# Kernel tuning notes

Hardware: AMD Instinct MI355X
Metric: run time of the kernel (lower is better)

The kernel has to match this reference:

```python
import jax, jax.numpy as jnp
import numpy as np

N, E, B, DIM, NF, EF, HID = 50000, 100000, 2000, 64, 14, 4, 128


def setup_inputs() -> dict:
    key = jax.random.key(0)
    ks = jax.random.split(key, 30)
    rn = lambda k, shape, scale: jax.random.normal(k, shape, jnp.float32) * scale
    inp = {}
    inp["x"] = rn(ks[0], (N, NF), 1.0)
    inp["edge_attr"] = jax.random.uniform(ks[1], (E, EF), jnp.float32)
    inp["edge_index"] = jax.random.randint(ks[2], (2, E), 0, N)
    # equal-size graphs: 25 nodes per graph, sorted segment ids
    inp["batch"] = (jnp.arange(N, dtype=jnp.int32) // (N // B)).astype(jnp.int32)
    inp["lin0_w"] = rn(ks[3], (DIM, NF), (1.0 / NF) ** 0.5)
    inp["lin0_b"] = jnp.zeros((DIM,), jnp.float32)
    inp["mlp_w1"] = rn(ks[4], (HID, EF), (1.0 / EF) ** 0.5)
    inp["mlp_b1"] = jnp.zeros((HID,), jnp.float32)
    inp["mlp_w2"] = rn(ks[5], (DIM * DIM, HID), (1.0 / HID) ** 0.5)
    inp["mlp_b2"] = jnp.zeros((DIM * DIM,), jnp.float32)
    inp["root"] = rn(ks[6], (DIM, DIM), (1.0 / DIM) ** 0.5)
    inp["conv_b"] = jnp.zeros((DIM,), jnp.float32)
    inp["gru_wih"] = rn(ks[7], (3 * DIM, DIM), (1.0 / DIM) ** 0.5)
    inp["gru_whh"] = rn(ks[8], (3 * DIM, DIM), (1.0 / DIM) ** 0.5)
    inp["gru_bih"] = jnp.zeros((3 * DIM,), jnp.float32)
    inp["gru_bhh"] = jnp.zeros((3 * DIM,), jnp.float32)
    inp["lstm_wih"] = rn(ks[9], (4 * DIM, 2 * DIM), (1.0 / (2 * DIM)) ** 0.5)
    inp["lstm_whh"] = rn(ks[10], (4 * DIM, DIM), (1.0 / DIM) ** 0.5)
    inp["lstm_bih"] = jnp.zeros((4 * DIM,), jnp.float32)
    inp["lstm_bhh"] = jnp.zeros((4 * DIM,), jnp.float32)
    inp["lin1_w"] = rn(ks[11], (DIM, 2 * DIM), (1.0 / (2 * DIM)) ** 0.5)
    inp["lin1_b"] = jnp.zeros((DIM,), jnp.float32)
    inp["lin2_w"] = rn(ks[12], (1, DIM), (1.0 / DIM) ** 0.5)
    inp["lin2_b"] = jnp.zeros((1,), jnp.float32)
    return inp


def _forward(x, edge_attr, edge_index, batch, lin0_w, lin0_b, mlp_w1, mlp_b1,
             mlp_w2, mlp_b2, root, conv_b, gru_wih, gru_whh, gru_bih, gru_bhh,
             lstm_wih, lstm_whh, lstm_bih, lstm_bhh, lin1_w, lin1_b, lin2_w, lin2_b):
    src, dst = edge_index[0], edge_index[1]
    n = x.shape[0]
    # edge MLP -> per-edge weight matrices [E, DIM, DIM]
    h_e = jax.nn.relu(edge_attr @ mlp_w1.T + mlp_b1)
    W_e = (h_e @ mlp_w2.T + mlp_b2).reshape(-1, DIM, DIM)
    deg = jnp.clip(jax.ops.segment_sum(jnp.ones_like(dst, jnp.float32), dst, n), 1.0)

    out = jax.nn.relu(x @ lin0_w.T + lin0_b)
    h = out  # GRU hidden (seq_len=1, 1 layer)
    for _ in range(3):
        msg = jnp.einsum('ei,eio->eo', out[src], W_e)  # per-edge matmul
        agg = jax.ops.segment_sum(msg, dst, n) / deg[:, None]  # scatter-mean
        m = jax.nn.relu(agg + out @ root + conv_b)  # NNConv: aggr + root + bias
        # GRU step
        gi = m @ gru_wih.T + gru_bih
        gh = h @ gru_whh.T + gru_bhh
        i_r, i_z, i_n = jnp.split(gi, 3, axis=-1)
        h_r, h_z, h_n = jnp.split(gh, 3, axis=-1)
        r = jax.nn.sigmoid(i_r + h_r)
        z = jax.nn.sigmoid(i_z + h_z)
        ng = jnp.tanh(i_n + r * h_n)
        h = (1.0 - z) * ng + z * h
        out = h

    # Set2Set pooling, 3 processing steps
    b = B
    qh = jnp.zeros((b, DIM), out.dtype)
    qc = jnp.zeros((b, DIM), out.dtype)
    q_star = jnp.zeros((b, 2 * DIM), out.dtype)
    for _ in range(3):
        gates = q_star @ lstm_wih.T + lstm_bih + qh @ lstm_whh.T + lstm_bhh
        gi_, gf_, gg_, go_ = jnp.split(gates, 4, axis=-1)
        qc = jax.nn.sigmoid(gf_) * qc + jax.nn.sigmoid(gi_) * jnp.tanh(gg_)
        qh = jax.nn.sigmoid(go_) * jnp.tanh(qc)
        q = qh
        e = jnp.sum(out * q[batch], axis=-1)  # [N]
        e_max = jax.ops.segment_max(e, batch, b)
        a = jnp.exp(e - e_max[batch])
        denom = jax.ops.segment_sum(a, batch, b)
        a = a / denom[batch]
        r_read = jax.ops.segment_sum(a[:, None] * out, batch, b)
        q_star = jnp.concatenate([q, r_read], axis=-1)

    y = jax.nn.relu(q_star @ lin1_w.T + lin1_b)
    y = y @ lin2_w.T + lin2_b
    return y.reshape(-1)


def reference(x, edge_attr, edge_index, batch, lin0_w, lin0_b, mlp_w1, mlp_b1,
              mlp_w2, mlp_b2, root, conv_b, gru_wih, gru_whh, gru_bih, gru_bhh,
              lstm_wih, lstm_whh, lstm_bih, lstm_bhh, lin1_w, lin1_b, lin2_w, lin2_b):
    return _forward(x, edge_attr, edge_index, batch, lin0_w, lin0_b, mlp_w1, mlp_b1,
                    mlp_w2, mlp_b2, root, conv_b, gru_wih, gru_whh, gru_bih, gru_bhh,
                    lstm_wih, lstm_whh, lstm_bih, lstm_bhh, lin1_w, lin1_b, lin2_w, lin2_b)
```

## Files before the change

### kernel.cpp

```cpp
#include <hip/hip_runtime.h>
#include <hip/hip_bf16.h>

#define NN 50000
#define EE 100000
#define BB 2000
#define DIM 64
#define NF 14
#define EF 4
#define HID 128
#define EPAD 100096

typedef __attribute__((ext_vector_type(8))) _Float16 half8;
typedef __attribute__((ext_vector_type(4))) _Float16 half4;
typedef __attribute__((ext_vector_type(4))) float floatx4;

__device__ __forceinline__ void async16(const _Float16* g, _Float16* l) {
    __builtin_amdgcn_global_load_lds(
        (const __attribute__((address_space(1))) unsigned int*)g,
        (__attribute__((address_space(3))) unsigned int*)l,
        16, 0, 0);
}

__global__ void prep_weights_kernel(
    const float* __restrict__ lih, const float* __restrict__ lhh, const float* __restrict__ l1,
    const float* __restrict__ root, const float* __restrict__ b2,
    const float* __restrict__ wih, const float* __restrict__ whh,
    const float* __restrict__ bih, const float* __restrict__ bhh,
    const float* __restrict__ w2,
    float* __restrict__ lihT, float* __restrict__ lhhT, float* __restrict__ l1T,
    _Float16* __restrict__ W1h, _Float16* __restrict__ W2h, float* __restrict__ fbias,
    _Float16* __restrict__ W2rT) {
    int t = blockIdx.x * 256 + threadIdx.x;
    if (t < 64 * 8192) {
        int o = t >> 13, k = t & 8191, i = k >> 7, h = k & 127;
        W2rT[(size_t)o * 8192 + k] = (_Float16)w2[(size_t)(i * 64 + o) * 128 + h];
    }
    if (t < 256 * 128) { int j = t / 128, k = t % 128; lihT[k * 256 + j] = lih[t]; }
    if (t < 256 * 64) { int j = t / 64, k = t % 64; lhhT[k * 256 + j] = lhh[t]; }
    if (t < 64 * 128) { int d = t / 128, k = t % 128; l1T[k * 64 + d] = l1[t]; }
    if (t < 64 * 128) {
        int n = t >> 7, k = t & 127;
        W1h[t] = (_Float16)(k < 64 ? root[k * 64 + n] : b2[(size_t)(k - 64) * 64 + n]);
    }
    if (t < 256 * 128) {
        int n2 = t >> 7, k = t & 127;
        int g = n2 >> 6, j = n2 & 63;
        float v;
        if (g == 0)      v = (k < 64) ? wih[j * 64 + k]         : whh[j * 64 + (k - 64)];
        else if (g == 1) v = (k < 64) ? wih[(64 + j) * 64 + k]  : whh[(64 + j) * 64 + (k - 64)];
        else if (g == 2) v = (k < 64) ? wih[(128 + j) * 64 + k] : 0.f;
        else             v = (k < 64) ? 0.f                     : whh[(128 + j) * 64 + (k - 64)];
        W2h[t] = (_Float16)v;
    }
    if (t < 256) {
        int g = t >> 6, j = t & 63;
        float v = (g == 0) ? bih[j] + bhh[j]
                : (g == 1) ? bih[64 + j] + bhh[64 + j]
                : (g == 2) ? bih[128 + j] : bhh[128 + j];
        fbias[t] = v;
    }
}

__global__ void prep_ne_kernel(const float* __restrict__ ea, const float* __restrict__ w1,
                               const float* __restrict__ b1, _Float16* __restrict__ he,
                               const float* __restrict__ x, const float* __restrict__ l0w,
                               const float* __restrict__ l0b, float* __restrict__ hv,
                               const int* __restrict__ ei, float* __restrict__ deg) {
    int t = blockIdx.x * 256 + threadIdx.x;
    if (t < EPAD * 128) {
        int el = t >> 7, h = t & 127;
        float acc = 0.f;
        if (el < EE) {
            const float4 a = *(const float4*)(ea + (size_t)el * 4);
            const float4 w = *(const float4*)(w1 + h * 4);
            acc = fmaxf(b1[h] + a.x * w.x + a.y * w.y + a.z * w.z + a.w * w.w, 0.f);
        }
        he[t] = (_Float16)acc;
    }
    if (t < NN * 64) {
        int n = t >> 6, d = t & 63;
        float acc = l0b[d];
        #pragma unroll
        for (int f = 0; f < NF; f++) acc += x[n * NF + f] * l0w[d * NF + f];
        hv[t] = fmaxf(acc, 0.f);
    }
    if (t < EE) atomicAdd(&deg[ei[EE + t]], 1.0f);
}

__global__ __launch_bounds__(256, 2) void msg_gemm_kernel(
    const float* __restrict__ hv, const _Float16* __restrict__ he16,
    const _Float16* __restrict__ W2rT, const int* __restrict__ ei,
    float* __restrict__ agg, float* __restrict__ xsum) {
    __shared__ _Float16 sB[2][16 * 64 * 8];
    __shared__ _Float16 sXs[256 * 72];
    __shared__ int sDst[256];
    const int t = threadIdx.x;
    const int eb = blockIdx.x * 256;
    const int lane = t & 63;
    const int w = t >> 6;
    const int col = lane & 15;
    const int quad = lane >> 4;

    if (t < 256) {
        int e = eb + t;
        sDst[t] = (e < EE) ? ei[EE + e] : 0;
    }
    #pragma unroll 4
    for (int rep = 0; rep < 16; rep++) {
        int idx = rep * 256 + t;
        int el = idx >> 4, d4 = idx & 15;
        int e = eb + el;
        float4 v = {0.f, 0.f, 0.f, 0.f};
        if (e < EE) {
            int src = ei[e];
            v = *(const float4*)(hv + (size_t)src * 64 + d4 * 4);
        }
        half4 h4 = {(_Float16)v.x, (_Float16)v.y, (_Float16)v.z, (_Float16)v.w};
        *(half4*)&sXs[el * 72 + d4 * 4] = h4;
    }
    __syncthreads();

    #pragma unroll 4
    for (int rep = 0; rep < 64; rep++) {
        int idx = rep * 256 + t;
        int el = idx >> 6, d = idx & 63;
        if (eb + el < EE)
            atomicAdd(&xsum[(size_t)sDst[el] * 64 + d], (float)sXs[el * 72 + d]);
    }

    half8 heReg[4][4];
    #pragma unroll
    for (int mt = 0; mt < 4; mt++) {
        int row = eb + w * 64 + mt * 16 + col;
        #pragma unroll
        for (int p = 0; p < 4; p++)
            heReg[mt][p] = *(const half8*)(he16 + (size_t)row * 128 + p * 32 + quad * 8);
    }

    floatx4 Cacc[4][4];
    #pragma unroll
    for (int mt = 0; mt < 4; mt++)
        #pragma unroll
        for (int nt = 0; nt < 4; nt++)
            Cacc[mt][nt] = (floatx4){0.f, 0.f, 0.f, 0.f};

    const _Float16* gsrc = W2rT + (size_t)(w * 16 + col) * 8192 + quad * 8;
    #pragma unroll
    for (int rep = 0; rep < 4; rep++)
        async16(gsrc + rep * 32, &sB[0][((w * 4 + rep) * 64 + lane) * 8]);
    __syncthreads();

    #pragma unroll 1
    for (int i4 = 0; i4 < 16; i4++) {
        half4 xsv[4];
        #pragma unroll
        for (int mt = 0; mt < 4; mt++)
            xsv[mt] = *(const half4*)&sXs[(w * 64 + mt * 16 + col) * 72 + i4 * 4];
        #pragma unroll
        for (int ii = 0; ii < 4; ii++) {
            const int i = i4 * 4 + ii;
            const int buf = i & 1;
            if (i < 63) {
                #pragma unroll
                for (int rep = 0; rep < 4; rep++)
                    async16(gsrc + (size_t)(i + 1) * 128 + rep * 32,
                            &sB[buf ^ 1][((w * 4 + rep) * 64 + lane) * 8]);
            }
            #pragma unroll
            for (int ks = 0; ks < 4; ks++) {
                half8 bfr[4];
                #pragma unroll
                for (int nt = 0; nt < 4; nt++)
                    bfr[nt] = *(const half8*)&sB[buf][((nt * 4 + ks) * 64 + lane) * 8];
                #pragma unroll
                for (int mt = 0; mt < 4; mt++) {
                    half8 afr = heReg[mt][ks] * xsv[mt][ii];
                    #pragma unroll
                    for (int nt = 0; nt < 4; nt++)
                        Cacc[mt][nt] = __builtin_amdgcn_mfma_f32_16x16x32_f16(afr, bfr[nt], Cacc[mt][nt], 0, 0, 0);
                }
            }
            __syncthreads();
        }
    }

    #pragma unroll
    for (int mt = 0; mt < 4; mt++) {
        #pragma unroll
        for (int r = 0; r < 4; r++) {
            int el = w * 64 + mt * 16 + quad * 4 + r;
            if (eb + el < EE) {
                float* ap = agg + (size_t)sDst[el] * 64 + col;
                #pragma unroll
                for (int nt = 0; nt < 4; nt++)
                    atomicAdd(ap + nt * 16, Cacc[mt][nt][r]);
            }
        }
    }
}

__global__ __launch_bounds__(256, 2) void node_fused_kernel(
    const float* __restrict__ hv_in, float* __restrict__ agg,
    float* __restrict__ xsum, const float* __restrict__ deg,
    const _Float16* __restrict__ W1h, const _Float16* __restrict__ W2h,
    const float* __restrict__ fbias, const float* __restrict__ cb,
    float* __restrict__ hv_out) {
    __shared__ _Float16 sA1[64 * 136];
    __shared__ _Float16 sA2[64 * 136];
    __shared__ float sH[64 * 68];
    __shared__ float sAgg[64 * 68];
    const int t = threadIdx.x;
    const int nb = blockIdx.x * 64;
    const int n = t >> 2, part = t & 3;
    {
        int gn = nb + n;
        bool valid = gn < NN;
        float inv = 1.f;
        if (valid) inv = 1.f / fmaxf(deg[gn], 1.f);
        #pragma unroll
        for (int c4 = 0; c4 < 4; c4++) {
            int d0 = part * 16 + c4 * 4;
            float4 hvv = {0.f, 0.f, 0.f, 0.f}, agv = {0.f, 0.f, 0.f, 0.f}, xsv = {0.f, 0.f, 0.f, 0.f};
            if (valid) {
                hvv = *(const float4*)(hv_in + (size_t)gn * 64 + d0);
                agv = *(const float4*)(agg + (size_t)gn * 64 + d0);
                xsv = *(const float4*)(xsum + (size_t)gn * 64 + d0);
            }
            agv.x *= inv; agv.y *= inv; agv.z *= inv; agv.w *= inv;
            xsv.x *= inv; xsv.y *= inv; xsv.z *= inv; xsv.w *= inv;
            half4 hvh = {(_Float16)hvv.x, (_Float16)hvv.y, (_Float16)hvv.z, (_Float16)hvv.w};
            half4 xsh = {(_Float16)xsv.x, (_Float16)xsv.y, (_Float16)xsv.z, (_Float16)xsv.w};
            *(half4*)&sA1[n * 136 + d0] = hvh;
            *(half4*)&sA1[n * 136 + 64 + d0] = xsh;
            *(half4*)&sA2[n * 136 + 64 + d0] = hvh;
            *(float4*)&sH[n * 68 + d0] = hvv;
            *(float4*)&sAgg[n * 68 + d0] = agv;
        }
        if (valid) {
            float4 z = {0.f, 0.f, 0.f, 0.f};
            #pragma unroll
            for (int c4 = 0; c4 < 4; c4++) {
                int d0 = part * 16 + c4 * 4;
                *(float4*)(agg + (size_t)gn * 64 + d0) = z;
                *(float4*)(xsum + (size_t)gn * 64 + d0) = z;
            }
        }
    }
    __syncthreads();

    const int lane = t & 63, w = t >> 6;
    const int col = lane & 15, quad = lane >> 4;

    floatx4 C1[4];
    #pragma unroll
    for (int nt = 0; nt < 4; nt++) {
        float b = cb[nt * 16 + col];
        C1[nt] = (floatx4){b, b, b, b};
    }
    #pragma unroll
    for (int ks = 0; ks < 4; ks++) {
        half8 a = *(const half8*)&sA1[(w * 16 + col) * 136 + ks * 32 + quad * 8];
        #pragma unroll
        for (int nt = 0; nt < 4; nt++) {
            half8 bfr = *(const half8*)(W1h + (size_t)(nt * 16 + col) * 128 + ks * 32 + quad * 8);
            C1[nt] = __builtin_amdgcn_mfma_f32_16x16x32_f16(a, bfr, C1[nt], 0, 0, 0);
        }
    }
    #pragma unroll
    for (int nt = 0; nt < 4; nt++) {
        #pragma unroll
        for (int r = 0; r < 4; r++) {
            int node = w * 16 + quad * 4 + r;
            int j = nt * 16 + col;
            float m = fmaxf(C1[nt][r] + sAgg[node * 68 + j], 0.f);
            sA2[node * 136 + j] = (_Float16)m;
        }
    }
    __syncthreads();

    floatx4 C2[16];
    #pragma unroll
    for (int nt2 = 0; nt2 < 16; nt2++) {
        float b = fbias[nt2 * 16 + col];
        C2[nt2] = (floatx4){b, b, b, b};
    }
    #pragma unroll
    for (int ks = 0; ks < 4; ks++) {
        half8 a = *(const half8*)&sA2[(w * 16 + col) * 136 + ks * 32 + quad * 8];
        #pragma unroll
        for (int nt2 = 0; nt2 < 16; nt2++) {
            half8 bfr = *(const half8*)(W2h + (size_t)(nt2 * 16 + col) * 128 + ks * 32 + quad * 8);
            C2[nt2] = __builtin_amdgcn_mfma_f32_16x16x32_f16(a, bfr, C2[nt2], 0, 0, 0);
        }
    }
    float hnew[4][4];
    #pragma unroll
    for (int r = 0; r < 4; r++) {
        int node = w * 16 + quad * 4 + r;
        #pragma unroll
        for (int jt = 0; jt < 4; jt++) {
            int j = jt * 16 + col;
            float rr = 1.f / (1.f + expf(-C2[jt][r]));
            float zz = 1.f / (1.f + expf(-C2[4 + jt][r]));
            float ng = tanhf(C2[8 + jt][r] + rr * C2[12 + jt][r]);
            float hold = sH[node * 68 + j];
            hnew[r][jt] = (1.f - zz) * ng + zz * hold;
        }
    }
    __syncthreads();
    #pragma unroll
    for (int r = 0; r < 4; r++) {
        int node = w * 16 + quad * 4 + r;
        #pragma unroll
        for (int jt = 0; jt < 4; jt++)
            sH[node * 68 + jt * 16 + col] = hnew[r][jt];
    }
    __syncthreads();
    {
        int gn = nb + n;
        if (gn < NN) {
            #pragma unroll
            for (int c4 = 0; c4 < 4; c4++) {
                int d0 = part * 16 + c4 * 4;
                *(float4*)(hv_out + (size_t)gn * 64 + d0) = *(const float4*)&sH[n * 68 + d0];
            }
        }
    }
}

__global__ __launch_bounds__(256) void set2set_kernel(
    const float* __restrict__ hv,
    const float* __restrict__ lihT, const float* __restrict__ lhhT,
    const float* __restrict__ l_bih, const float* __restrict__ l_bhh,
    const float* __restrict__ lin1T, const float* __restrict__ lin1_b,
    const float* __restrict__ lin2_w, const float* __restrict__ lin2_b,
    float* __restrict__ out) {
    __shared__ float outS[25 * 65];
    __shared__ float qs[128], qh[64], qc[64], gat[256], ew[32], aw[32], red[64];
    int g = blockIdx.x;
    int t = threadIdx.x;
    for (int p = t; p < 25 * 64; p += 256) {
        int j = p >> 6, i = p & 63;
        outS[j * 65 + i] = hv[(size_t)(g * 25 + j) * 64 + i];
    }
    if (t < 128) qs[t] = 0.f;
    if (t < 64) { qh[t] = 0.f; qc[t] = 0.f; }
    __syncthreads();
    for (int it = 0; it < 3; it++) {
        float acc = l_bih[t] + l_bhh[t];
        for (int k = 0; k < 128; k++) acc += qs[k] * lihT[k * 256 + t];
        for (int k = 0; k < 64; k++) acc += qh[k] * lhhT[k * 256 + t];
        gat[t] = acc;
        __syncthreads();
        if (t < 64) {
            float ig = 1.f / (1.f + expf(-gat[t]));
            float fg = 1.f / (1.f + expf(-gat[64 + t]));
            float gg = tanhf(gat[128 + t]);
            float og = 1.f / (1.f + expf(-gat[192 + t]));
            float c = fg * qc[t] + ig * gg;
            qc[t] = c;
            qh[t] = og * tanhf(c);
        }
        __syncthreads();
        if (t < 25) {
            float e = 0.f;
            for (int i = 0; i < 64; i++) e += outS[t * 65 + i] * qh[i];
            ew[t] = e;
        }
        __syncthreads();
        if (t == 0) {
            float mx = ew[0];
            for (int j = 1; j < 25; j++) mx = fmaxf(mx, ew[j]);
            float s = 0.f;
            for (int j = 0; j < 25; j++) { float a = expf(ew[j] - mx); aw[j] = a; s += a; }
            float inv = 1.f / s;
            for (int j = 0; j < 25; j++) aw[j] *= inv;
        }
        __syncthreads();
        if (t < 64) {
            float r = 0.f;
            for (int j = 0; j < 25; j++) r += aw[j] * outS[j * 65 + t];
            qs[t] = qh[t];
            qs[64 + t] = r;
        }
        __syncthreads();
    }
    if (t < 64) {
        float y1 = lin1_b[t];
        for (int k = 0; k < 128; k++) y1 += qs[k] * lin1T[k * 64 + t];
        y1 = fmaxf(y1, 0.f);
        red[t] = y1 * lin2_w[t];
    }
    __syncthreads();
    if (t == 0) {
        float y = lin2_b[0];
        for (int i = 0; i < 64; i++) y += red[i];
        out[g] = y;
    }
}

extern "C" void kernel_launch(void* const* d_in, const int* in_sizes, int n_in,
                              void* d_out, int out_size, void* d_ws, size_t ws_size,
                              hipStream_t stream) {
    const float* x        = (const float*)d_in[0];
    const float* ea       = (const float*)d_in[1];
    const int*   ei       = (const int*)  d_in[2];
    const float* lin0_w   = (const float*)d_in[4];
    const float* lin0_b   = (const float*)d_in[5];
    const float* mlp_w1   = (const float*)d_in[6];
    const float* mlp_b1   = (const float*)d_in[7];
    const float* mlp_w2   = (const float*)d_in[8];
    const float* mlp_b2   = (const float*)d_in[9];
    const float* root     = (const float*)d_in[10];
    const float* conv_b   = (const float*)d_in[11];
    const float* gru_wih  = (const float*)d_in[12];
    const float* gru_whh  = (const float*)d_in[13];
    const float* gru_bih  = (const float*)d_in[14];
    const float* gru_bhh  = (const float*)d_in[15];
    const float* lstm_wih = (const float*)d_in[16];
    const float* lstm_whh = (const float*)d_in[17];
    const float* lstm_bih = (const float*)d_in[18];
    const float* lstm_bhh = (const float*)d_in[19];
    const float* lin1_w   = (const float*)d_in[20];
    const float* lin1_b   = (const float*)d_in[21];
    const float* lin2_w   = (const float*)d_in[22];
    const float* lin2_b   = (const float*)d_in[23];
    float* out = (float*)d_out;

    char* base = (char*)d_ws;
    size_t off = 0;
    auto carve = [&](size_t bytes) -> void* {
        void* r = base + off;
        off = (off + bytes + 255) & ~(size_t)255;
        return r;
    };
    float* hv   = (float*)carve((size_t)NN * 64 * 4);
    float* agg  = (float*)carve((size_t)NN * 64 * 4);
    float* xsum = (float*)carve((size_t)NN * 64 * 4);
    float* deg  = (float*)carve((size_t)NN * 4);
    float* lihT = (float*)carve(128 * 256 * 4);
    float* lhhT = (float*)carve(64 * 256 * 4);
    float* l1T  = (float*)carve(128 * 64 * 4);
    float* fbias = (float*)carve(256 * 4);
    _Float16* he16 = (_Float16*)carve((size_t)EPAD * 128 * 2);
    _Float16* W2rT = (_Float16*)carve((size_t)64 * 8192 * 2);
    _Float16* W1h  = (_Float16*)carve((size_t)64 * 128 * 2);
    _Float16* W2h  = (_Float16*)carve((size_t)256 * 128 * 2);

    hipMemsetAsync(agg, 0, (size_t)NN * 64 * 4 * 2 + (size_t)NN * 4, stream);
    prep_weights_kernel<<<2048, 256, 0, stream>>>(lstm_wih, lstm_whh, lin1_w,
                                                  root, mlp_b2, gru_wih, gru_whh, gru_bih, gru_bhh,
                                                  mlp_w2, lihT, lhhT, l1T, W1h, W2h, fbias, W2rT);
    prep_ne_kernel<<<(EPAD * 128 + 255) / 256, 256, 0, stream>>>(ea, mlp_w1, mlp_b1, he16,
                                                                 x, lin0_w, lin0_b, hv, ei, deg);

    for (int it = 0; it < 3; it++) {
        msg_gemm_kernel<<<EPAD / 256, 256, 0, stream>>>(hv, he16, W2rT, ei, agg, xsum);
        node_fused_kernel<<<(NN + 63) / 64, 256, 0, stream>>>(hv, agg, xsum, deg,
                                                              W1h, W2h, fbias, conv_b, hv);
    }

    set2set_kernel<<<BB, 256, 0, stream>>>(hv, lihT, lhhT, lstm_bih, lstm_bhh,
                                           l1T, lin1_b, lin2_w, lin2_b, out);
}
```

Measured before the change: 813.8 us.

## Retile message GEMM warps to 128 edges by 32 columns with register-staged B loads

Each wave now covers 128 edges and 32 output columns instead of 64 edges and 64 columns. The weight loads change from global-to-LDS async copies to ordinary register prefetch, written to the other LDS buffer after the MFMAs run. The xsum atomic scatter moves after the GEMM, and the barrier before the he loads is dropped. This changes per-wave register use (heReg doubles), the LDS read pattern and the B-fragment reuse, and adds register pressure and possible occupancy loss under launch_bounds(256,2).

New measurement: 843.3 us. 3.6% more time.

```diff
diff --git a/kernel.cpp b/kernel.cpp
--- a/kernel.cpp
+++ b/kernel.cpp
@@ -13,13 +13,6 @@
 typedef __attribute__((ext_vector_type(8))) _Float16 half8;
 typedef __attribute__((ext_vector_type(4))) _Float16 half4;
 typedef __attribute__((ext_vector_type(4))) float floatx4;
-
-__device__ __forceinline__ void async16(const _Float16* g, _Float16* l) {
-    __builtin_amdgcn_global_load_lds(
-        (const __attribute__((address_space(1))) unsigned int*)g,
-        (__attribute__((address_space(3))) unsigned int*)l,
-        16, 0, 0);
-}
 
 __global__ void prep_weights_kernel(
     const float* __restrict__ lih, const float* __restrict__ lhh, const float* __restrict__ l1,
@@ -100,6 +93,8 @@
     const int w = t >> 6;
     const int col = lane & 15;
     const int quad = lane >> 4;
+    const int eh = w >> 1;
+    const int cg = w & 1;
 
     if (t < 256) {
         int e = eb + t;
@@ -118,84 +113,92 @@
         half4 h4 = {(_Float16)v.x, (_Float16)v.y, (_Float16)v.z, (_Float16)v.w};
         *(half4*)&sXs[el * 72 + d4 * 4] = h4;
     }
-    __syncthreads();
-
+
+    half8 heReg[8][4];
+    #pragma unroll
+    for (int mt = 0; mt < 8; mt++) {
+        int row = eb + eh * 128 + mt * 16 + col;
+        #pragma unroll
+        for (int p = 0; p < 4; p++)
+            heReg[mt][p] = *(const half8*)(he16 + (size_t)row * 128 + p * 32 + quad * 8);
+    }
+
+    floatx4 Cacc[8][2];
+    #pragma unroll
+    for (int mt = 0; mt < 8; mt++)
+        #pragma unroll
+        for (int nt = 0; nt < 2; nt++)
+            Cacc[mt][nt] = (floatx4){0.f, 0.f, 0.f, 0.f};
+
+    const _Float16* gsrc = W2rT + (size_t)((w >> 1) * 32 + (w & 1) * 16 + col) * 8192 + quad * 8;
+    half8 pre[4];
+    {
+        #pragma unroll
+        for (int rep = 0; rep < 4; rep++)
+            pre[rep] = *(const half8*)(gsrc + rep * 32);
+        #pragma unroll
+        for (int rep = 0; rep < 4; rep++)
+            *(half8*)&sB[0][((w * 4 + rep) * 64 + lane) * 8] = pre[rep];
+    }
+    __syncthreads();
+
+    #pragma unroll 1
+    for (int i4 = 0; i4 < 16; i4++) {
+        half4 xsv[8];
+        #pragma unroll
+        for (int mt = 0; mt < 8; mt++)
+            xsv[mt] = *(const half4*)&sXs[(eh * 128 + mt * 16 + col) * 72 + i4 * 4];
+        #pragma unroll
+        for (int ii = 0; ii < 4; ii++) {
+            const int i = i4 * 4 + ii;
+            const int buf = i & 1;
+            if (i < 63) {
+                #pragma unroll
+                for (int rep = 0; rep < 4; rep++)
+                    pre[rep] = *(const half8*)(gsrc + (size_t)(i + 1) * 128 + rep * 32);
+            }
+            #pragma unroll
+            for (int ks = 0; ks < 4; ks++) {
+                half8 bfr[2];
+                #pragma unroll
+                for (int nt = 0; nt < 2; nt++)
+                    bfr[nt] = *(const half8*)&sB[buf][((cg * 8 + nt * 4 + ks) * 64 + lane) * 8];
+                #pragma unroll
+                for (int mt = 0; mt < 8; mt++) {
+                    half8 afr = heReg[mt][ks] * xsv[mt][ii];
+                    #pragma unroll
+                    for (int nt = 0; nt < 2; nt++)
+                        Cacc[mt][nt] = __builtin_amdgcn_mfma_f32_16x16x32_f16(afr, bfr[nt], Cacc[mt][nt], 0, 0, 0);
+                }
+            }
+            if (i < 63) {
+                #pragma unroll
+                for (int rep = 0; rep < 4; rep++)
+                    *(half8*)&sB[buf ^ 1][((w * 4 + rep) * 64 + lane) * 8] = pre[rep];
+            }
+            __syncthreads();
+        }
+    }
+
+    #pragma unroll
+    for (int mt = 0; mt < 8; mt++) {
+        #pragma unroll
+        for (int r = 0; r < 4; r++) {
+            int el = eh * 128 + mt * 16 + quad * 4 + r;
+            if (eb + el < EE) {
+                float* ap = agg + (size_t)sDst[el] * 64 + cg * 32 + col;
+                #pragma unroll
+                for (int nt = 0; nt < 2; nt++)
+                    atomicAdd(ap + nt * 16, Cacc[mt][nt][r]);
+            }
+        }
+    }
     #pragma unroll 4
     for (int rep = 0; rep < 64; rep++) {
         int idx = rep * 256 + t;
         int el = idx >> 6, d = idx & 63;
         if (eb + el < EE)
             atomicAdd(&xsum[(size_t)sDst[el] * 64 + d], (float)sXs[el * 72 + d]);
-    }
-
-    half8 heReg[4][4];
-    #pragma unroll
-    for (int mt = 0; mt < 4; mt++) {
-        int row = eb + w * 64 + mt * 16 + col;
-        #pragma unroll
-        for (int p = 0; p < 4; p++)
-            heReg[mt][p] = *(const half8*)(he16 + (size_t)row * 128 + p * 32 + quad * 8);
-    }
-
-    floatx4 Cacc[4][4];
-    #pragma unroll
-    for (int mt = 0; mt < 4; mt++)
-        #pragma unroll
-        for (int nt = 0; nt < 4; nt++)
-            Cacc[mt][nt] = (floatx4){0.f, 0.f, 0.f, 0.f};
-
-    const _Float16* gsrc = W2rT + (size_t)(w * 16 + col) * 8192 + quad * 8;
-    #pragma unroll
-    for (int rep = 0; rep < 4; rep++)
-        async16(gsrc + rep * 32, &sB[0][((w * 4 + rep) * 64 + lane) * 8]);
-    __syncthreads();
-
-    #pragma unroll 1
-    for (int i4 = 0; i4 < 16; i4++) {
-        half4 xsv[4];
-        #pragma unroll
-        for (int mt = 0; mt < 4; mt++)
-            xsv[mt] = *(const half4*)&sXs[(w * 64 + mt * 16 + col) * 72 + i4 * 4];
-        #pragma unroll
-        for (int ii = 0; ii < 4; ii++) {
-            const int i = i4 * 4 + ii;
-            const int buf = i & 1;
-            if (i < 63) {
-                #pragma unroll
-                for (int rep = 0; rep < 4; rep++)
-                    async16(gsrc + (size_t)(i + 1) * 128 + rep * 32,
-                            &sB[buf ^ 1][((w * 4 + rep) * 64 + lane) * 8]);
-            }
-            #pragma unroll
-            for (int ks = 0; ks < 4; ks++) {
-                half8 bfr[4];
-                #pragma unroll
-                for (int nt = 0; nt < 4; nt++)
-                    bfr[nt] = *(const half8*)&sB[buf][((nt * 4 + ks) * 64 + lane) * 8];
-                #pragma unroll
-                for (int mt = 0; mt < 4; mt++) {
-                    half8 afr = heReg[mt][ks] * xsv[mt][ii];
-                    #pragma unroll
-                    for (int nt = 0; nt < 4; nt++)
-                        Cacc[mt][nt] = __builtin_amdgcn_mfma_f32_16x16x32_f16(afr, bfr[nt], Cacc[mt][nt], 0, 0, 0);
-                }
-            }
-            __syncthreads();
-        }
-    }
-
-    #pragma unroll
-    for (int mt = 0; mt < 4; mt++) {
-        #pragma unroll
-        for (int r = 0; r < 4; r++) {
-            int el = w * 64 + mt * 16 + quad * 4 + r;
-            if (eb + el < EE) {
-                float* ap = agg + (size_t)sDst[el] * 64 + col;
-                #pragma unroll
-                for (int nt = 0; nt < 4; nt++)
-                    atomicAdd(ap + nt * 16, Cacc[mt][nt][r]);
-            }
-        }
     }
 }
 
```

## Fuse all stages into one persistent megakernel with software grid barriers

Applied to the files above, without the earlier changes.

Replaces the memset, the two prep kernels, the three message/node iteration pairs and the set2set kernel with a single persistent kernel of 391 blocks. Stages are separated by an atomic-counter grid barrier, and preprocessing work is spread across the resident blocks with grid-stride loops. The aim is to remove repeated launch overhead and the idle gaps between kernels. Inside the message GEMM, the global_load_lds async copies are replaced by a register-staged prefetch, and the xsum atomics are moved after the GEMM. The trade-offs are the cost of the barriers, the need for every block to be co-resident, and lower parallelism in the prep and set2set phases.

Result: slower. 1.720 ms (+111.4%).

```diff
diff --git a/kernel.cpp b/kernel.cpp
--- a/kernel.cpp
+++ b/kernel.cpp
@@ -9,101 +9,60 @@
 #define EF 4
 #define HID 128
 #define EPAD 100096
+#define NBLK 391
+#define GSZ (NBLK * 256)
 
 typedef __attribute__((ext_vector_type(8))) _Float16 half8;
 typedef __attribute__((ext_vector_type(4))) _Float16 half4;
 typedef __attribute__((ext_vector_type(4))) float floatx4;
 
-__device__ __forceinline__ void async16(const _Float16* g, _Float16* l) {
-    __builtin_amdgcn_global_load_lds(
-        (const __attribute__((address_space(1))) unsigned int*)g,
-        (__attribute__((address_space(3))) unsigned int*)l,
-        16, 0, 0);
-}
-
-__global__ void prep_weights_kernel(
-    const float* __restrict__ lih, const float* __restrict__ lhh, const float* __restrict__ l1,
-    const float* __restrict__ root, const float* __restrict__ b2,
-    const float* __restrict__ wih, const float* __restrict__ whh,
-    const float* __restrict__ bih, const float* __restrict__ bhh,
-    const float* __restrict__ w2,
-    float* __restrict__ lihT, float* __restrict__ lhhT, float* __restrict__ l1T,
-    _Float16* __restrict__ W1h, _Float16* __restrict__ W2h, float* __restrict__ fbias,
-    _Float16* __restrict__ W2rT) {
-    int t = blockIdx.x * 256 + threadIdx.x;
-    if (t < 64 * 8192) {
-        int o = t >> 13, k = t & 8191, i = k >> 7, h = k & 127;
-        W2rT[(size_t)o * 8192 + k] = (_Float16)w2[(size_t)(i * 64 + o) * 128 + h];
-    }
-    if (t < 256 * 128) { int j = t / 128, k = t % 128; lihT[k * 256 + j] = lih[t]; }
-    if (t < 256 * 64) { int j = t / 64, k = t % 64; lhhT[k * 256 + j] = lhh[t]; }
-    if (t < 64 * 128) { int d = t / 128, k = t % 128; l1T[k * 64 + d] = l1[t]; }
-    if (t < 64 * 128) {
-        int n = t >> 7, k = t & 127;
-        W1h[t] = (_Float16)(k < 64 ? root[k * 64 + n] : b2[(size_t)(k - 64) * 64 + n]);
-    }
-    if (t < 256 * 128) {
-        int n2 = t >> 7, k = t & 127;
-        int g = n2 >> 6, j = n2 & 63;
-        float v;
-        if (g == 0)      v = (k < 64) ? wih[j * 64 + k]         : whh[j * 64 + (k - 64)];
-        else if (g == 1) v = (k < 64) ? wih[(64 + j) * 64 + k]  : whh[(64 + j) * 64 + (k - 64)];
-        else if (g == 2) v = (k < 64) ? wih[(128 + j) * 64 + k] : 0.f;
-        else             v = (k < 64) ? 0.f                     : whh[(128 + j) * 64 + (k - 64)];
-        W2h[t] = (_Float16)v;
-    }
-    if (t < 256) {
-        int g = t >> 6, j = t & 63;
-        float v = (g == 0) ? bih[j] + bhh[j]
-                : (g == 1) ? bih[64 + j] + bhh[64 + j]
-                : (g == 2) ? bih[128 + j] : bhh[128 + j];
-        fbias[t] = v;
-    }
-}
-
-__global__ void prep_ne_kernel(const float* __restrict__ ea, const float* __restrict__ w1,
-                               const float* __restrict__ b1, _Float16* __restrict__ he,
-                               const float* __restrict__ x, const float* __restrict__ l0w,
-                               const float* __restrict__ l0b, float* __restrict__ hv,
-                               const int* __restrict__ ei, float* __restrict__ deg) {
-    int t = blockIdx.x * 256 + threadIdx.x;
-    if (t < EPAD * 128) {
-        int el = t >> 7, h = t & 127;
-        float acc = 0.f;
-        if (el < EE) {
-            const float4 a = *(const float4*)(ea + (size_t)el * 4);
-            const float4 w = *(const float4*)(w1 + h * 4);
-            acc = fmaxf(b1[h] + a.x * w.x + a.y * w.y + a.z * w.z + a.w * w.w, 0.f);
-        }
-        he[t] = (_Float16)acc;
-    }
-    if (t < NN * 64) {
-        int n = t >> 6, d = t & 63;
-        float acc = l0b[d];
-        #pragma unroll
-        for (int f = 0; f < NF; f++) acc += x[n * NF + f] * l0w[d * NF + f];
-        hv[t] = fmaxf(acc, 0.f);
-    }
-    if (t < EE) atomicAdd(&deg[ei[EE + t]], 1.0f);
-}
-
-__global__ __launch_bounds__(256, 2) void msg_gemm_kernel(
-    const float* __restrict__ hv, const _Float16* __restrict__ he16,
-    const _Float16* __restrict__ W2rT, const int* __restrict__ ei,
-    float* __restrict__ agg, float* __restrict__ xsum) {
-    __shared__ _Float16 sB[2][16 * 64 * 8];
-    __shared__ _Float16 sXs[256 * 72];
-    __shared__ int sDst[256];
+struct MegaP {
+    const float* x; const float* ea; const int* ei;
+    const float* l0w; const float* l0b;
+    const float* w1; const float* b1;
+    const float* w2; const float* b2;
+    const float* root; const float* cb;
+    const float* gwih; const float* gwhh; const float* gbih; const float* gbhh;
+    const float* lih; const float* lhh; const float* lbih; const float* lbhh;
+    const float* l1; const float* l1b; const float* l2w; const float* l2b;
+    float* hv; float* agg; float* xsum; float* deg;
+    float* lihT; float* lhhT; float* l1T; float* fbias;
+    _Float16* he16; _Float16* W2rT; _Float16* W1h; _Float16* W2h;
+    int* bar;
+    float* out;
+};
+
+__device__ __forceinline__ void gbar(int* bar) {
+    __syncthreads();
+    if (threadIdx.x == 0) {
+        __threadfence();
+        int gen = __hip_atomic_load(&bar[1], __ATOMIC_RELAXED, __HIP_MEMORY_SCOPE_AGENT);
+        int prev = __hip_atomic_fetch_add(&bar[0], 1, __ATOMIC_ACQ_REL, __HIP_MEMORY_SCOPE_AGENT);
+        if (prev == NBLK - 1) {
+            __hip_atomic_store(&bar[0], 0, __ATOMIC_RELAXED, __HIP_MEMORY_SCOPE_AGENT);
+            __hip_atomic_store(&bar[1], gen + 1, __ATOMIC_RELEASE, __HIP_MEMORY_SCOPE_AGENT);
+        } else {
+            while (__hip_atomic_load(&bar[1], __ATOMIC_ACQUIRE, __HIP_MEMORY_SCOPE_AGENT) == gen)
+                __builtin_amdgcn_s_sleep(1);
+        }
+        __threadfence();
+    }
+    __syncthreads();
+}
+
+__device__ __forceinline__ void msg_body(const MegaP& P, char* smem, int blk, bool it0) {
+    _Float16* sB  = (_Float16*)smem;
+    _Float16* sXs = (_Float16*)(smem + 32768);
+    int* sDst     = (int*)(smem + 69632);
     const int t = threadIdx.x;
-    const int eb = blockIdx.x * 256;
-    const int lane = t & 63;
-    const int w = t >> 6;
-    const int col = lane & 15;
-    const int quad = lane >> 4;
-
-    if (t < 256) {
+    const int eb = blk * 256;
+    const int lane = t & 63, w = t >> 6;
+    const int col = lane & 15, quad = lane >> 4;
+
+    {
         int e = eb + t;
-        sDst[t] = (e < EE) ? ei[EE + e] : 0;
+        sDst[t] = (e < EE) ? P.ei[EE + e] : 0;
+        if (it0 && e < EE) atomicAdd(&P.deg[sDst[t]], 1.0f);
     }
     #pragma unroll 4
     for (int rep = 0; rep < 16; rep++) {
@@ -112,21 +71,12 @@
         int e = eb + el;
         float4 v = {0.f, 0.f, 0.f, 0.f};
         if (e < EE) {
-            int src = ei[e];
-            v = *(const float4*)(hv + (size_t)src * 64 + d4 * 4);
+            int src = P.ei[e];
+            v = *(const float4*)(P.hv + (size_t)src * 64 + d4 * 4);
         }
         half4 h4 = {(_Float16)v.x, (_Float16)v.y, (_Float16)v.z, (_Float16)v.w};
         *(half4*)&sXs[el * 72 + d4 * 4] = h4;
     }
-    __syncthreads();
-
-    #pragma unroll 4
-    for (int rep = 0; rep < 64; rep++) {
-        int idx = rep * 256 + t;
-        int el = idx >> 6, d = idx & 63;
-        if (eb + el < EE)
-            atomicAdd(&xsum[(size_t)sDst[el] * 64 + d], (float)sXs[el * 72 + d]);
-    }
 
     half8 heReg[4][4];
     #pragma unroll
@@ -134,7 +84,7 @@
         int row = eb + w * 64 + mt * 16 + col;
         #pragma unroll
         for (int p = 0; p < 4; p++)
-            heReg[mt][p] = *(const half8*)(he16 + (size_t)row * 128 + p * 32 + quad * 8);
+            heReg[mt][p] = *(const half8*)(P.he16 + (size_t)row * 128 + p * 32 + quad * 8);
     }
 
     floatx4 Cacc[4][4];
@@ -144,10 +94,16 @@
         for (int nt = 0; nt < 4; nt++)
             Cacc[mt][nt] = (floatx4){0.f, 0.f, 0.f, 0.f};
 
-    const _Float16* gsrc = W2rT + (size_t)(w * 16 + col) * 8192 + quad * 8;
-    #pragma unroll
-    for (int rep = 0; rep < 4; rep++)
-        async16(gsrc + rep * 32, &sB[0][((w * 4 + rep) * 64 + lane) * 8]);
+    const _Float16* gsrc = P.W2rT + (size_t)(w * 16 + col) * 8192 + quad * 8;
+    half8 pre[4];
+    {
+        #pragma unroll
+        for (int rep = 0; rep < 4; rep++)
+            pre[rep] = *(const half8*)(gsrc + rep * 32);
+        #pragma unroll
+        for (int rep = 0; rep < 4; rep++)
+            *(half8*)&sB[((w * 4 + rep) * 64 + lane) * 8] = pre[rep];
+    }
     __syncthreads();
 
     #pragma unroll 1
@@ -163,15 +119,14 @@
             if (i < 63) {
                 #pragma unroll
                 for (int rep = 0; rep < 4; rep++)
-                    async16(gsrc + (size_t)(i + 1) * 128 + rep * 32,
-                            &sB[buf ^ 1][((w * 4 + rep) * 64 + lane) * 8]);
+                    pre[rep] = *(const half8*)(gsrc + (size_t)(i + 1) * 128 + rep * 32);
             }
             #pragma unroll
             for (int ks = 0; ks < 4; ks++) {
                 half8 bfr[4];
                 #pragma unroll
                 for (int nt = 0; nt < 4; nt++)
-                    bfr[nt] = *(const half8*)&sB[buf][((nt * 4 + ks) * 64 + lane) * 8];
+                    bfr[nt] = *(const half8*)&sB[(size_t)buf * 8192 + ((nt * 4 + ks) * 64 + lane) * 8];
                 #pragma unroll
                 for (int mt = 0; mt < 4; mt++) {
                     half8 afr = heReg[mt][ks] * xsv[mt][ii];
@@ -180,6 +135,11 @@
                         Cacc[mt][nt] = __builtin_amdgcn_mfma_f32_16x16x32_f16(afr, bfr[nt], Cacc[mt][nt], 0, 0, 0);
                 }
             }
+            if (i < 63) {
+                #pragma unroll
+                for (int rep = 0; rep < 4; rep++)
+                    *(half8*)&sB[(size_t)(buf ^ 1) * 8192 + ((w * 4 + rep) * 64 + lane) * 8] = pre[rep];
+            }
             __syncthreads();
         }
     }
@@ -190,41 +150,43 @@
         for (int r = 0; r < 4; r++) {
             int el = w * 64 + mt * 16 + quad * 4 + r;
             if (eb + el < EE) {
-                float* ap = agg + (size_t)sDst[el] * 64 + col;
+                float* ap = P.agg + (size_t)sDst[el] * 64 + col;
                 #pragma unroll
                 for (int nt = 0; nt < 4; nt++)
                     atomicAdd(ap + nt * 16, Cacc[mt][nt][r]);
             }
         }
     }
-}
-
-__global__ __launch_bounds__(256, 2) void node_fused_kernel(
-    const float* __restrict__ hv_in, float* __restrict__ agg,
-    float* __restrict__ xsum, const float* __restrict__ deg,
-    const _Float16* __restrict__ W1h, const _Float16* __restrict__ W2h,
-    const float* __restrict__ fbias, const float* __restrict__ cb,
-    float* __restrict__ hv_out) {
-    __shared__ _Float16 sA1[64 * 136];
-    __shared__ _Float16 sA2[64 * 136];
-    __shared__ float sH[64 * 68];
-    __shared__ float sAgg[64 * 68];
+    #pragma unroll 4
+    for (int rep = 0; rep < 64; rep++) {
+        int idx = rep * 256 + t;
+        int el = idx >> 6, d = idx & 63;
+        if (eb + el < EE)
+            atomicAdd(&P.xsum[(size_t)sDst[el] * 64 + d], (float)sXs[el * 72 + d]);
+    }
+}
+
+__device__ __forceinline__ void node_body(const MegaP& P, char* smem, int nb) {
+    _Float16* sA1 = (_Float16*)smem;
+    _Float16* sA2 = (_Float16*)(smem + 17408);
+    float* sH     = (float*)(smem + 34816);
+    float* sAgg   = (float*)(smem + 52224);
     const int t = threadIdx.x;
-    const int nb = blockIdx.x * 64;
+    __syncthreads();
     const int n = t >> 2, part = t & 3;
     {
         int gn = nb + n;
         bool valid = gn < NN;
         float inv = 1.f;
-        if (valid) inv = 1.f / fmaxf(deg[gn], 1.f);
+        if (valid) inv = 1.f / fmaxf(P.deg[gn], 1.f);
         #pragma unroll
         for (int c4 = 0; c4 < 4; c4++) {
             int d0 = part * 16 + c4 * 4;
             float4 hvv = {0.f, 0.f, 0.f, 0.f}, agv = {0.f, 0.f, 0.f, 0.f}, xsv = {0.f, 0.f, 0.f, 0.f};
             if (valid) {
-                hvv = *(const float4*)(hv_in + (size_t)gn * 64 + d0);
-                agv = *(const float4*)(agg + (size_t)gn * 64 + d0);
-                xsv = *(const float4*)(xsum + (size_t)gn * 64 + d0);
+                hvv = *(const float4*)(P.hv + (size_t)gn * 64 + d0);
+                agv = *(const float4*)(P.agg + (size_t)gn * 64 + d0);
+                xsv = *(const float4*)(P.xsum + (size_t)gn * 64 + d0);
             }
             agv.x *= inv; agv.y *= inv; agv.z *= inv; agv.w *= inv;
             xsv.x *= inv; xsv.y *= inv; xsv.z *= inv; xsv.w *= inv;
@@ -241,8 +203,8 @@
             #pragma unroll
             for (int c4 = 0; c4 < 4; c4++) {
                 int d0 = part * 16 + c4 * 4;
-                *(float4*)(agg + (size_t)gn * 64 + d0) = z;
-                *(float4*)(xsum + (size_t)gn * 64 + d0) = z;
+                *(float4*)(P.agg + (size_t)gn * 64 + d0) = z;
+                *(float4*)(P.xsum + (size_t)gn * 64 + d0) = z;
             }
         }
     }
@@ -254,7 +216,7 @@
     floatx4 C1[4];
     #pragma unroll
     for (int nt = 0; nt < 4; nt++) {
-        float b = cb[nt * 16 + col];
+        float b = P.cb[nt * 16 + col];
         C1[nt] = (floatx4){b, b, b, b};
     }
     #pragma unroll
@@ -262,7 +224,7 @@
         half8 a = *(const half8*)&sA1[(w * 16 + col) * 136 + ks * 32 + quad * 8];
         #pragma unroll
         for (int nt = 0; nt < 4; nt++) {
-            half8 bfr = *(const half8*)(W1h + (size_t)(nt * 16 + col) * 128 + ks * 32 + quad * 8);
+            half8 bfr = *(const half8*)(P.W1h + (size_t)(nt * 16 + col) * 128 + ks * 32 + quad * 8);
             C1[nt] = __builtin_amdgcn_mfma_f32_16x16x32_f16(a, bfr, C1[nt], 0, 0, 0);
         }
     }
@@ -281,7 +243,7 @@
     floatx4 C2[16];
     #pragma unroll
     for (int nt2 = 0; nt2 < 16; nt2++) {
-        float b = fbias[nt2 * 16 + col];
+        float b = P.fbias[nt2 * 16 + col];
         C2[nt2] = (floatx4){b, b, b, b};
     }
     #pragma unroll
@@ -289,7 +251,7 @@
         half8 a = *(const half8*)&sA2[(w * 16 + col) * 136 + ks * 32 + quad * 8];
         #pragma unroll
         for (int nt2 = 0; nt2 < 16; nt2++) {
-            half8 bfr = *(const half8*)(W2h + (size_t)(nt2 * 16 + col) * 128 + ks * 32 + quad * 8);
+            half8 bfr = *(const half8*)(P.W2h + (size_t)(nt2 * 16 + col) * 128 + ks * 32 + quad * 8);
             C2[nt2] = __builtin_amdgcn_mfma_f32_16x16x32_f16(a, bfr, C2[nt2], 0, 0, 0);
         }
     }
@@ -322,34 +284,34 @@
             #pragma unroll
             for (int c4 = 0; c4 < 4; c4++) {
                 int d0 = part * 16 + c4 * 4;
-                *(float4*)(hv_out + (size_t)gn * 64 + d0) = *(const float4*)&sH[n * 68 + d0];
-            }
-        }
-    }
-}
-
-__global__ __launch_bounds__(256) void set2set_kernel(
-    const float* __restrict__ hv,
-    const float* __restrict__ lihT, const float* __restrict__ lhhT,
-    const float* __restrict__ l_bih, const float* __restrict__ l_bhh,
-    const float* __restrict__ lin1T, const float* __restrict__ lin1_b,
-    const float* __restrict__ lin2_w, const float* __restrict__ lin2_b,
-    float* __restrict__ out) {
-    __shared__ float outS[25 * 65];
-    __shared__ float qs[128], qh[64], qc[64], gat[256], ew[32], aw[32], red[64];
-    int g = blockIdx.x;
-    int t = threadIdx.x;
+                *(float4*)(P.hv + (size_t)gn * 64 + d0) = *(const float4*)&sH[n * 68 + d0];
+            }
+        }
+    }
+}
+
+__device__ __forceinline__ void set2set_body(const MegaP& P, char* smem, int g) {
+    float* outS = (float*)smem;
+    float* qs  = (float*)smem + 1632;
+    float* qh  = (float*)smem + 1760;
+    float* qc  = (float*)smem + 1824;
+    float* gat = (float*)smem + 1888;
+    float* ew  = (float*)smem + 2144;
+    float* aw  = (float*)smem + 2176;
+    float* red = (float*)smem + 2208;
+    const int t = threadIdx.x;
+    __syncthreads();
     for (int p = t; p < 25 * 64; p += 256) {
         int j = p >> 6, i = p & 63;
-        outS[j * 65 + i] = hv[(size_t)(g * 25 + j) * 64 + i];
+        outS[j * 65 + i] = P.hv[(size_t)(g * 25 + j) * 64 + i];
     }
     if (t < 128) qs[t] = 0.f;
     if (t < 64) { qh[t] = 0.f; qc[t] = 0.f; }
     __syncthreads();
     for (int it = 0; it < 3; it++) {
-        float acc = l_bih[t] + l_bhh[t];
-        for (int k = 0; k < 128; k++) acc += qs[k] * lihT[k * 256 + t];
-        for (int k = 0; k < 64; k++) acc += qh[k] * lhhT[k * 256 + t];
+        float acc = P.lbih[t] + P.lbhh[t];
+        for (int k = 0; k < 128; k++) acc += qs[k] * P.lihT[k * 256 + t];
+        for (int k = 0; k < 64; k++) acc += qh[k] * P.lhhT[k * 256 + t];
         gat[t] = acc;
         __syncthreads();
         if (t < 64) {
@@ -386,47 +348,95 @@
         __syncthreads();
     }
     if (t < 64) {
-        float y1 = lin1_b[t];
-        for (int k = 0; k < 128; k++) y1 += qs[k] * lin1T[k * 64 + t];
+        float y1 = P.l1b[t];
+        for (int k = 0; k < 128; k++) y1 += qs[k] * P.l1T[k * 64 + t];
         y1 = fmaxf(y1, 0.f);
-        red[t] = y1 * lin2_w[t];
+        red[t] = y1 * P.l2w[t];
     }
     __syncthreads();
     if (t == 0) {
-        float y = lin2_b[0];
+        float y = P.l2b[0];
         for (int i = 0; i < 64; i++) y += red[i];
-        out[g] = y;
-    }
+        P.out[g] = y;
+    }
+}
+
+__global__ __launch_bounds__(256, 2) void mega_kernel(MegaP P) {
+    __shared__ __align__(16) char smem[70656];
+    const int blk = blockIdx.x;
+    const int t = threadIdx.x;
+    const int gtid = blk * 256 + t;
+
+    {
+        float4 z4 = {0.f, 0.f, 0.f, 0.f};
+        float4* agz = (float4*)P.agg;
+        for (int i = gtid; i < (NN * 64 * 2) / 4; i += GSZ) agz[i] = z4;
+        for (int i = gtid; i < NN; i += GSZ) P.deg[i] = 0.f;
+
+        for (int i = gtid; i < 64 * 8192; i += GSZ) {
+            int o = i >> 13, k = i & 8191, ii = k >> 7, h = k & 127;
+            P.W2rT[i] = (_Float16)P.w2[(size_t)(ii * 64 + o) * 128 + h];
+        }
+        if (gtid < 256 * 128) { int j = gtid / 128, k = gtid % 128; P.lihT[k * 256 + j] = P.lih[gtid]; }
+        if (gtid < 256 * 64)  { int j = gtid / 64, k = gtid % 64;  P.lhhT[k * 256 + j] = P.lhh[gtid]; }
+        if (gtid < 64 * 128)  { int d = gtid / 128, k = gtid % 128; P.l1T[k * 64 + d] = P.l1[gtid]; }
+        if (gtid < 64 * 128) {
+            int n = gtid >> 7, k = gtid & 127;
+            P.W1h[gtid] = (_Float16)(k < 64 ? P.root[k * 64 + n] : P.b2[(size_t)(k - 64) * 64 + n]);
+        }
+        if (gtid < 256 * 128) {
+            int n2 = gtid >> 7, k = gtid & 127;
+            int gg = n2 >> 6, j = n2 & 63;
+            float v;
+            if (gg == 0)      v = (k < 64) ? P.gwih[j * 64 + k]         : P.gwhh[j * 64 + (k - 64)];
+            else if (gg == 1) v = (k < 64) ? P.gwih[(64 + j) * 64 + k]  : P.gwhh[(64 + j) * 64 + (k - 64)];
+            else if (gg == 2) v = (k < 64) ? P.gwih[(128 + j) * 64 + k] : 0.f;
+            else              v = (k < 64) ? 0.f                        : P.gwhh[(128 + j) * 64 + (k - 64)];
+            P.W2h[gtid] = (_Float16)v;
+        }
+        if (gtid < 256) {
+            int gg = gtid >> 6, j = gtid & 63;
+            float v = (gg == 0) ? P.gbih[j] + P.gbhh[j]
+                    : (gg == 1) ? P.gbih[64 + j] + P.gbhh[64 + j]
+                    : (gg == 2) ? P.gbih[128 + j] : P.gbhh[128 + j];
+            P.fbias[gtid] = v;
+        }
+        const int eb = blk * 256;
+        for (int r = t; r < 256 * 128; r += 256) {
+            int el = eb + (r >> 7), h = r & 127;
+            float acc = 0.f;
+            if (el < EE) {
+                float4 a = *(const float4*)(P.ea + (size_t)el * 4);
+                float4 wv = *(const float4*)(P.w1 + h * 4);
+                acc = fmaxf(P.b1[h] + a.x * wv.x + a.y * wv.y + a.z * wv.z + a.w * wv.w, 0.f);
+            }
+            P.he16[(size_t)el * 128 + h] = (_Float16)acc;
+        }
+        for (int i = gtid; i < NN * 64; i += GSZ) {
+            int n = i >> 6, d = i & 63;
+            float acc = P.l0b[d];
+            #pragma unroll
+            for (int f = 0; f < NF; f++) acc += P.x[n * NF + f] * P.l0w[d * NF + f];
+            P.hv[i] = fmaxf(acc, 0.f);
+        }
+    }
+    gbar(P.bar);
+
+    for (int it = 0; it < 3; it++) {
+        msg_body(P, smem, blk, it == 0);
+        gbar(P.bar);
+        node_body(P, smem, blk * 64);
+        node_body(P, smem, (blk + NBLK) * 64);
+        gbar(P.bar);
+    }
+
+    for (int g = blk; g < BB; g += NBLK)
+        set2set_body(P, smem, g);
 }
 
 extern "C" void kernel_launch(void* const* d_in, const int* in_sizes, int n_in,
                               void* d_out, int out_size, void* d_ws, size_t ws_size,
                               hipStream_t stream) {
-    const float* x        = (const float*)d_in[0];
-    const float* ea       = (const float*)d_in[1];
-    const int*   ei       = (const int*)  d_in[2];
-    const float* lin0_w   = (const float*)d_in[4];
-    const float* lin0_b   = (const float*)d_in[5];
-    const float* mlp_w1   = (const float*)d_in[6];
-    const float* mlp_b1   = (const float*)d_in[7];
-    const float* mlp_w2   = (const float*)d_in[8];
-    const float* mlp_b2   = (const float*)d_in[9];
-    const float* root     = (const float*)d_in[10];
-    const float* conv_b   = (const float*)d_in[11];
-    const float* gru_wih  = (const float*)d_in[12];
-    const float* gru_whh  = (const float*)d_in[13];
-    const float* gru_bih  = (const float*)d_in[14];
-    const float* gru_bhh  = (const float*)d_in[15];
-    const float* lstm_wih = (const float*)d_in[16];
-    const float* lstm_whh = (const float*)d_in[17];
-    const float* lstm_bih = (const float*)d_in[18];
-    const float* lstm_bhh = (const float*)d_in[19];
-    const float* lin1_w   = (const float*)d_in[20];
-    const float* lin1_b   = (const float*)d_in[21];
-    const float* lin2_w   = (const float*)d_in[22];
-    const float* lin2_b   = (const float*)d_in[23];
-    float* out = (float*)d_out;
-
     char* base = (char*)d_ws;
     size_t off = 0;
     auto carve = [&](size_t bytes) -> void* {
@@ -434,6 +444,7 @@
         off = (off + bytes + 255) & ~(size_t)255;
         return r;
     };
+    int*   bar  = (int*)carve(256);
     float* hv   = (float*)carve((size_t)NN * 64 * 4);
     float* agg  = (float*)carve((size_t)NN * 64 * 4);
     float* xsum = (float*)carve((size_t)NN * 64 * 4);
@@ -447,19 +458,36 @@
     _Float16* W1h  = (_Float16*)carve((size_t)64 * 128 * 2);
     _Float16* W2h  = (_Float16*)carve((size_t)256 * 128 * 2);
 
-    hipMemsetAsync(agg, 0, (size_t)NN * 64 * 4 * 2 + (size_t)NN * 4, stream);
-    prep_weights_kernel<<<2048, 256, 0, stream>>>(lstm_wih, lstm_whh, lin1_w,
-                                                  root, mlp_b2, gru_wih, gru_whh, gru_bih, gru_bhh,
-                                                  mlp_w2, lihT, lhhT, l1T, W1h, W2h, fbias, W2rT);
-    prep_ne_kernel<<<(EPAD * 128 + 255) / 256, 256, 0, stream>>>(ea, mlp_w1, mlp_b1, he16,
-                                                                 x, lin0_w, lin0_b, hv, ei, deg);
-
-    for (int it = 0; it < 3; it++) {
-        msg_gemm_kernel<<<EPAD / 256, 256, 0, stream>>>(hv, he16, W2rT, ei, agg, xsum);
-        node_fused_kernel<<<(NN + 63) / 64, 256, 0, stream>>>(hv, agg, xsum, deg,
-                                                              W1h, W2h, fbias, conv_b, hv);
-    }
-
-    set2set_kernel<<<BB, 256, 0, stream>>>(hv, lihT, lhhT, lstm_bih, lstm_bhh,
-                                           l1T, lin1_b, lin2_w, lin2_b, out);
-}
+    MegaP p;
+    p.x    = (const float*)d_in[0];
+    p.ea   = (const float*)d_in[1];
+    p.ei   = (const int*)  d_in[2];
+    p.l0w  = (const float*)d_in[4];
+    p.l0b  = (const float*)d_in[5];
+    p.w1   = (const float*)d_in[6];
+    p.b1   = (const float*)d_in[7];
+    p.w2   = (const float*)d_in[8];
+    p.b2   = (const float*)d_in[9];
+    p.root = (const float*)d_in[10];
+    p.cb   = (const float*)d_in[11];
+    p.gwih = (const float*)d_in[12];
+    p.gwhh = (const float*)d_in[13];
+    p.gbih = (const float*)d_in[14];
+    p.gbhh = (const float*)d_in[15];
+    p.lih  = (const float*)d_in[16];
+    p.lhh  = (const float*)d_in[17];
+    p.lbih = (const float*)d_in[18];
+    p.lbhh = (const float*)d_in[19];
+    p.l1   = (const float*)d_in[20];
+    p.l1b  = (const float*)d_in[21];
+    p.l2w  = (const float*)d_in[22];
+    p.l2b  = (const float*)d_in[23];
+    p.hv = hv; p.agg = agg; p.xsum = xsum; p.deg = deg;
+    p.lihT = lihT; p.lhhT = lhhT; p.l1T = l1T; p.fbias = fbias;
+    p.he16 = he16; p.W2rT = W2rT; p.W1h = W1h; p.W2h = W2h;
+    p.bar = bar;
+    p.out = (float*)d_out;
+
+    hipMemsetAsync(bar, 0, 256, stream);
+    mega_kernel<<<NBLK, 256, 0, stream>>>(p);
+}
```
